# Kernel tuning notes

Measured on AMD Instinct MI355X. Metric: run time of the kernel, lower is better.

## Reference

```python
import jax, jax.numpy as jnp
import numpy as np

B, N, T, H, P = 512, 128, 336, 32, 1  # batch, nodes, seq_len, hidden, pred_len


def setup_inputs() -> dict:
    key = jax.random.key(0)
    ks = jax.random.split(key, 9)
    s = 1.0 / np.sqrt(H)  # torch LSTM/Linear init bound
    u = lambda k, shape: jax.random.uniform(k, shape, dtype=jnp.float32, minval=-s, maxval=s)
    return {
        "x": jax.random.normal(ks[0], (B, N, T), dtype=jnp.float32),
        # layer 0: input_size=1
        "W_ih0": u(ks[1], (N, 4 * H, 1)),
        "W_hh0": u(ks[2], (N, 4 * H, H)),
        "b0": u(ks[3], (N, 4 * H)),  # = b_ih0 + b_hh0 (additive in the cell)
        # layer 1: input_size=H
        "W_ih1": u(ks[4], (N, 4 * H, H)),
        "W_hh1": u(ks[5], (N, 4 * H, H)),
        "b1": u(ks[6], (N, 4 * H)),
        # per-node linear head
        "W_fc": u(ks[7], (N, P, H)),
        "b_fc": u(ks[8], (N, P)),
    }


def _cell(x_proj, h, c, W_hh, b):
    # x_proj, h, c: [B, N, H*(...)]; torch gate order: i, f, g, o
    gates = x_proj + jnp.einsum("bnh,ngh->bng", h, W_hh) + b
    i, f, g, o = jnp.split(gates, 4, axis=-1)
    c = jax.nn.sigmoid(f) * c + jax.nn.sigmoid(i) * jnp.tanh(g)
    h = jax.nn.sigmoid(o) * jnp.tanh(c)
    return h, c


def reference(x, W_ih0, W_hh0, b0, W_ih1, W_hh1, b1, W_fc, b_fc):
    Bx, Nx, Tx = x.shape
    Hx = W_hh0.shape[-1]
    Wi0 = W_ih0[:, :, 0]  # [N, 4H] since input_size == 1
    xs = jnp.moveaxis(x, 2, 0)  # [T, B, N]
    zeros = jnp.zeros((Bx, Nx, Hx), x.dtype)
    init = (zeros, zeros, zeros, zeros)  # h0, c0, h1, c1

    def step(carry, x_t):
        h0, c0, h1, c1 = carry
        xp0 = x_t[:, :, None] * Wi0[None]          # [B, N, 4H]
        h0, c0 = _cell(xp0, h0, c0, W_hh0, b0)
        xp1 = jnp.einsum("bnh,ngh->bng", h0, W_ih1)
        h1, c1 = _cell(xp1, h1, c1, W_hh1, b1)
        return (h0, c0, h1, c1), None

    (h0, c0, h1, c1), _ = jax.lax.scan(step, init, xs)
    # last-timestep top-layer hidden through per-node linear head
    return jnp.einsum("bnh,nph->bnp", h1, W_fc) + b_fc[None]
```

## Files before the change

### kernel.cpp

```cpp
#include <hip/hip_runtime.h>
#include <stdint.h>

#define NB 512
#define NN 128
#define NT 336
#define NH 32
#define NG 128

typedef short bf16x8 __attribute__((ext_vector_type(8)));
typedef float f32x4  __attribute__((ext_vector_type(4)));
typedef float f32x2  __attribute__((ext_vector_type(2)));
typedef float f32v4  __attribute__((ext_vector_type(4)));

#define LOG2E 1.4426950408889634f

__device__ __forceinline__ f32x2 exp2v(f32x2 v) {
  f32x2 r; r.x = __builtin_amdgcn_exp2f(v.x); r.y = __builtin_amdgcn_exp2f(v.y); return r;
}
__device__ __forceinline__ f32x2 rcpv(f32x2 v) {
  f32x2 r; r.x = __builtin_amdgcn_rcpf(v.x); r.y = __builtin_amdgcn_rcpf(v.y); return r;
}
__device__ __forceinline__ short f2bf(float f) {
  unsigned u = __builtin_bit_cast(unsigned, f) + 0x8000u;
  return (short)(u >> 16);
}

template<bool BIAS>
__device__ __forceinline__ f32x2 cell_pair(f32x2 gi, f32x2 gf, f32x2 gg, f32x2 go,
                                           f32x2& cst, float ebi, float ebf,
                                           float ebg, float ebo) {
  f32x2 wi = exp2v(gi), wf = exp2v(gf), uu = exp2v(gg), wo = exp2v(go);
  f32x2 Ai, Af, Au, Ao, nu;
  if (BIAS) {
    Ai = wi * ebi + 1.0f;
    Af = wf * ebf + 1.0f;
    Au = uu * ebg + 1.0f;
    Ao = wo * ebo + 1.0f;
    nu = 1.0f - uu * ebg;
  } else {
    Ai = wi + 1.0f; Af = wf + 1.0f; Au = uu + 1.0f; Ao = wo + 1.0f;
    nu = 1.0f - uu;
  }
  f32x2 P  = Ai * Au;
  f32x2 N  = cst * P + nu * Af;
  f32x2 cn = N * rcpv(Af * P);
  cst = cn;
  f32x2 sarg = cn * (-2.0f * LOG2E);
  sarg.x = fminf(sarg.x, 80.0f);
  sarg.y = fminf(sarg.y, 80.0f);
  f32x2 vv = exp2v(sarg);
  f32x2 hh = (1.0f - vv) * rcpv(Ao * (vv + 1.0f));
  return hh;
}

__global__ __launch_bounds__(256, 2) void lstm_kernel(
    const float* __restrict__ x,
    const float* __restrict__ Wih0,
    const float* __restrict__ Whh0,
    const float* __restrict__ b0,
    const float* __restrict__ Wih1,
    const float* __restrict__ Whh1,
    const float* __restrict__ b1,
    const float* __restrict__ Wfc,
    const float* __restrict__ bfc,
    float* __restrict__ out)
{
  const int tid  = threadIdx.x;
  const int wave = tid >> 6;
  const int lane = tid & 63;
  const int c    = lane & 15;
  const int q    = lane >> 4;
  const int n    = blockIdx.x >> 3;
  const int m0   = ((blockIdx.x & 7) * 4 + wave) * 16;

  __shared__ short lds[4 * 2 * 16 * 40];
  short* my0 = lds + wave * (2 * 16 * 40);
  short* my1 = my0 + 16 * 40;

  const float sc_tab[8] = {-LOG2E, -LOG2E, -LOG2E, -LOG2E,
                           -2.0f * LOG2E, -2.0f * LOG2E, -LOG2E, -LOG2E};

  bf16x8 wb0[8], wb1[8], wb2[8];
  {
    const float* pW0 = Whh0 + n * (NG * NH);
    const float* pW1 = Wih1 + n * (NG * NH);
    const float* pW2 = Whh1 + n * (NG * NH);
#pragma unroll
    for (int tau = 0; tau < 8; ++tau) {
      int off = (tau * 16 + c) * NH + q * 8;
      float sc = sc_tab[tau];
#pragma unroll
      for (int j = 0; j < 8; ++j) {
        wb0[tau][j] = f2bf(sc * pW0[off + j]);
        wb1[tau][j] = f2bf(sc * pW1[off + j]);
        wb2[tau][j] = f2bf(sc * pW2[off + j]);
      }
    }
  }
  float b0g[8], eb1[8], wi0g[8];
#pragma unroll
  for (int tau = 0; tau < 8; ++tau) {
    int g = tau * 16 + c;
    float sc = sc_tab[tau];
    b0g[tau]  = sc * b0[n * NG + g];
    eb1[tau]  = __builtin_amdgcn_exp2f(sc * b1[n * NG + g]);
    wi0g[tau] = sc * Wih0[n * NG + g];
  }
  const float wfc0 = Wfc[n * NH + c];
  const float wfc1 = Wfc[n * NH + 16 + c];

  const float* px0 = x + ((size_t)(m0 + q * 4 + 0) * NN + n) * NT;
  const float* px1 = x + ((size_t)(m0 + q * 4 + 1) * NN + n) * NT;
  const float* px2 = x + ((size_t)(m0 + q * 4 + 2) * NN + n) * NT;
  const float* px3 = x + ((size_t)(m0 + q * 4 + 3) * NN + n) * NT;

  bf16x8 a0 = {0,0,0,0,0,0,0,0};
  bf16x8 a1 = {0,0,0,0,0,0,0,0};
  f32x2 c0p[2][2], c1p[2][2], h1p[2][2];
#pragma unroll
  for (int tu = 0; tu < 2; ++tu)
#pragma unroll
    for (int p = 0; p < 2; ++p) {
      c0p[tu][p] = (f32x2){0.f, 0.f};
      c1p[tu][p] = (f32x2){0.f, 0.f};
      h1p[tu][p] = (f32x2){0.f, 0.f};
    }

  const f32x4 zero4 = {0.f, 0.f, 0.f, 0.f};

#pragma unroll 1
  for (int t4 = 0; t4 < NT / 4; ++t4) {
    f32v4 xr0 = *(const f32v4*)(px0 + t4 * 4);
    f32v4 xr1 = *(const f32v4*)(px1 + t4 * 4);
    f32v4 xr2 = *(const f32v4*)(px2 + t4 * 4);
    f32v4 xr3 = *(const f32v4*)(px3 + t4 * 4);

#pragma unroll
    for (int ts = 0; ts < 4; ++ts) {
      f32x2 x01 = {xr0[ts], xr1[ts]};
      f32x2 x23 = {xr2[ts], xr3[ts]};

      f32x4 acc[8];
#pragma unroll
      for (int tau = 0; tau < 8; ++tau) {
        f32x2 w2 = {wi0g[tau], wi0g[tau]};
        f32x2 b2 = {b0g[tau], b0g[tau]};
        f32x2 lo = x01 * w2 + b2;
        f32x2 hi = x23 * w2 + b2;
        acc[tau] = (f32x4){lo.x, lo.y, hi.x, hi.y};
      }
#pragma unroll
      for (int tau = 0; tau < 8; ++tau)
        acc[tau] = __builtin_amdgcn_mfma_f32_16x16x32_bf16(a0, wb0[tau], acc[tau], 0, 0, 0);

#pragma unroll
      for (int tu = 0; tu < 2; ++tu) {
#pragma unroll
        for (int p = 0; p < 2; ++p) {
          f32x2 gi = { acc[tu    ][2*p], acc[tu    ][2*p+1] };
          f32x2 gf = { acc[tu + 2][2*p], acc[tu + 2][2*p+1] };
          f32x2 gg = { acc[tu + 4][2*p], acc[tu + 4][2*p+1] };
          f32x2 go = { acc[tu + 6][2*p], acc[tu + 6][2*p+1] };
          f32x2 hh = cell_pair<false>(gi, gf, gg, go, c0p[tu][p], 1.f, 1.f, 1.f, 1.f);
          my0[(q * 4 + 2*p    ) * 40 + tu * 16 + c] = f2bf(hh.x);
          my0[(q * 4 + 2*p + 1) * 40 + tu * 16 + c] = f2bf(hh.y);
        }
      }
      asm volatile("" ::: "memory");
      a0 = *(const bf16x8*)(my0 + c * 40 + q * 8);

#pragma unroll
      for (int tau = 0; tau < 8; ++tau)
        acc[tau] = __builtin_amdgcn_mfma_f32_16x16x32_bf16(a0, wb1[tau], zero4, 0, 0, 0);
#pragma unroll
      for (int tau = 0; tau < 8; ++tau)
        acc[tau] = __builtin_amdgcn_mfma_f32_16x16x32_bf16(a1, wb2[tau], acc[tau], 0, 0, 0);

#pragma unroll
      for (int tu = 0; tu < 2; ++tu) {
#pragma unroll
        for (int p = 0; p < 2; ++p) {
          f32x2 gi = { acc[tu    ][2*p], acc[tu    ][2*p+1] };
          f32x2 gf = { acc[tu + 2][2*p], acc[tu + 2][2*p+1] };
          f32x2 gg = { acc[tu + 4][2*p], acc[tu + 4][2*p+1] };
          f32x2 go = { acc[tu + 6][2*p], acc[tu + 6][2*p+1] };
          f32x2 hh = cell_pair<true>(gi, gf, gg, go, c1p[tu][p],
                                     eb1[tu], eb1[tu + 2], eb1[tu + 4], eb1[tu + 6]);
          h1p[tu][p] = hh;
          my1[(q * 4 + 2*p    ) * 40 + tu * 16 + c] = f2bf(hh.x);
          my1[(q * 4 + 2*p + 1) * 40 + tu * 16 + c] = f2bf(hh.y);
        }
      }
      asm volatile("" ::: "memory");
      a1 = *(const bf16x8*)(my1 + c * 40 + q * 8);
    }
  }

  float s0 = h1p[0][0].x * wfc0 + h1p[1][0].x * wfc1;
  float s1 = h1p[0][0].y * wfc0 + h1p[1][0].y * wfc1;
  float s2 = h1p[0][1].x * wfc0 + h1p[1][1].x * wfc1;
  float s3 = h1p[0][1].y * wfc0 + h1p[1][1].y * wfc1;
#pragma unroll
  for (int off = 1; off < 16; off <<= 1) {
    s0 += __shfl_xor(s0, off, 64);
    s1 += __shfl_xor(s1, off, 64);
    s2 += __shfl_xor(s2, off, 64);
    s3 += __shfl_xor(s3, off, 64);
  }
  if (c < 4) {
    float v = (c == 0) ? s0 : (c == 1) ? s1 : (c == 2) ? s2 : s3;
    out[(size_t)(m0 + q * 4 + c) * NN + n] = v + bfc[n];
  }
}

extern "C" void kernel_launch(void* const* d_in, const int* in_sizes, int n_in,
                              void* d_out, int out_size, void* d_ws, size_t ws_size,
                              hipStream_t stream) {
  const float* x    = (const float*)d_in[0];
  const float* Wih0 = (const float*)d_in[1];
  const float* Whh0 = (const float*)d_in[2];
  const float* b0   = (const float*)d_in[3];
  const float* Wih1 = (const float*)d_in[4];
  const float* Whh1 = (const float*)d_in[5];
  const float* b1   = (const float*)d_in[6];
  const float* Wfc  = (const float*)d_in[7];
  const float* bfc  = (const float*)d_in[8];
  float* out = (float*)d_out;

  lstm_kernel<<<dim3(1024), dim3(256), 0, stream>>>(
      x, Wih0, Whh0, b0, Wih1, Whh1, b1, Wfc, bfc, out);
}
```

Measured before the change: 1.301 ms.

## Transpose MFMA operands to keep hidden state in registers, drop LDS round-trip

The recurrent matmuls are reformulated so that weights are the A operand and hidden state the B operand. Each lane's packed bf16 hidden outputs then directly form the next step's operand, which removes the per-step LDS store/load transpose for both layers. The layer-0 input projection and bias are folded into an extra MFMA using split hi/lo bf16 encodings, and the layer-1 bias is used as the accumulator init instead of exp-scaled factors. This adds MFMA work per step and relies on a specific weight K-permutation matching the output layout; correctness depends on that mapping.

Result: slower. 1.329 ms (+2.2%).

```diff
diff --git a/kernel.cpp b/kernel.cpp
--- a/kernel.cpp
+++ b/kernel.cpp
@@ -11,6 +11,7 @@
 typedef float f32x4  __attribute__((ext_vector_type(4)));
 typedef float f32x2  __attribute__((ext_vector_type(2)));
 typedef float f32v4  __attribute__((ext_vector_type(4)));
+typedef unsigned int u32x4 __attribute__((ext_vector_type(4)));
 
 #define LOG2E 1.4426950408889634f
 
@@ -24,23 +25,17 @@
   unsigned u = __builtin_bit_cast(unsigned, f) + 0x8000u;
   return (short)(u >> 16);
 }
-
-template<bool BIAS>
+__device__ __forceinline__ unsigned cvtpk(float a, float b) {
+  unsigned r;
+  asm("v_cvt_pk_bf16_f32 %0, %1, %2" : "=v"(r) : "v"(a), "v"(b));
+  return r;
+}
+
 __device__ __forceinline__ f32x2 cell_pair(f32x2 gi, f32x2 gf, f32x2 gg, f32x2 go,
-                                           f32x2& cst, float ebi, float ebf,
-                                           float ebg, float ebo) {
+                                           f32x2& cst) {
   f32x2 wi = exp2v(gi), wf = exp2v(gf), uu = exp2v(gg), wo = exp2v(go);
-  f32x2 Ai, Af, Au, Ao, nu;
-  if (BIAS) {
-    Ai = wi * ebi + 1.0f;
-    Af = wf * ebf + 1.0f;
-    Au = uu * ebg + 1.0f;
-    Ao = wo * ebo + 1.0f;
-    nu = 1.0f - uu * ebg;
-  } else {
-    Ai = wi + 1.0f; Af = wf + 1.0f; Au = uu + 1.0f; Ao = wo + 1.0f;
-    nu = 1.0f - uu;
-  }
+  f32x2 Ai = wi + 1.0f, Af = wf + 1.0f, Au = uu + 1.0f, Ao = wo + 1.0f;
+  f32x2 nu = 1.0f - uu;
   f32x2 P  = Ai * Au;
   f32x2 N  = cst * P + nu * Af;
   f32x2 cn = N * rcpv(Af * P);
@@ -72,10 +67,7 @@
   const int q    = lane >> 4;
   const int n    = blockIdx.x >> 3;
   const int m0   = ((blockIdx.x & 7) * 4 + wave) * 16;
-
-  __shared__ short lds[4 * 2 * 16 * 40];
-  short* my0 = lds + wave * (2 * 16 * 40);
-  short* my1 = my0 + 16 * 40;
+  const int row  = m0 + c;
 
   const float sc_tab[8] = {-LOG2E, -LOG2E, -LOG2E, -LOG2E,
                            -2.0f * LOG2E, -2.0f * LOG2E, -LOG2E, -LOG2E};
@@ -87,72 +79,89 @@
     const float* pW2 = Whh1 + n * (NG * NH);
 #pragma unroll
     for (int tau = 0; tau < 8; ++tau) {
-      int off = (tau * 16 + c) * NH + q * 8;
       float sc = sc_tab[tau];
+      int rowoff = (tau * 16 + c) * NH;
 #pragma unroll
       for (int j = 0; j < 8; ++j) {
-        wb0[tau][j] = f2bf(sc * pW0[off + j]);
-        wb1[tau][j] = f2bf(sc * pW1[off + j]);
-        wb2[tau][j] = f2bf(sc * pW2[off + j]);
+        int k = (j < 4) ? (q * 4 + j) : (16 + q * 4 + (j - 4));
+        wb0[tau][j] = f2bf(sc * pW0[rowoff + k]);
+        wb1[tau][j] = f2bf(sc * pW1[rowoff + k]);
+        wb2[tau][j] = f2bf(sc * pW2[rowoff + k]);
       }
     }
   }
-  float b0g[8], eb1[8], wi0g[8];
+
+  bf16x8 a2[8];
+  {
+    const bf16x8 z8 = {0,0,0,0,0,0,0,0};
+#pragma unroll
+    for (int tau = 0; tau < 8; ++tau) {
+      float sc = sc_tab[tau];
+      int g = tau * 16 + c;
+      float Wv = sc * Wih0[n * NG + g];
+      unsigned Wb = __builtin_bit_cast(unsigned, Wv) & 0xFFFF0000u;
+      float Bv = sc * b0[n * NG + g];
+      unsigned Bb = __builtin_bit_cast(unsigned, Bv) & 0xFFFF0000u;
+      bf16x8 t;
+      t[0] = (short)(Wb >> 16);
+      t[1] = t[0];
+      t[2] = f2bf(Wv - __builtin_bit_cast(float, Wb));
+      t[3] = (short)(Bb >> 16);
+      t[4] = f2bf(Bv - __builtin_bit_cast(float, Bb));
+      t[5] = 0; t[6] = 0; t[7] = 0;
+      a2[tau] = (q == 0) ? t : z8;
+    }
+  }
+
+  f32x4 b1g4[8];
 #pragma unroll
   for (int tau = 0; tau < 8; ++tau) {
-    int g = tau * 16 + c;
     float sc = sc_tab[tau];
-    b0g[tau]  = sc * b0[n * NG + g];
-    eb1[tau]  = __builtin_amdgcn_exp2f(sc * b1[n * NG + g]);
-    wi0g[tau] = sc * Wih0[n * NG + g];
-  }
-  const float wfc0 = Wfc[n * NH + c];
-  const float wfc1 = Wfc[n * NH + 16 + c];
-
-  const float* px0 = x + ((size_t)(m0 + q * 4 + 0) * NN + n) * NT;
-  const float* px1 = x + ((size_t)(m0 + q * 4 + 1) * NN + n) * NT;
-  const float* px2 = x + ((size_t)(m0 + q * 4 + 2) * NN + n) * NT;
-  const float* px3 = x + ((size_t)(m0 + q * 4 + 3) * NN + n) * NT;
-
-  bf16x8 a0 = {0,0,0,0,0,0,0,0};
-  bf16x8 a1 = {0,0,0,0,0,0,0,0};
-  f32x2 c0p[2][2], c1p[2][2], h1p[2][2];
+#pragma unroll
+    for (int r = 0; r < 4; ++r)
+      b1g4[tau][r] = sc * b1[n * NG + tau * 16 + q * 4 + r];
+  }
+
+  const float* px = x + ((size_t)row * NN + n) * NT;
+
+  bf16x8 h0f = {0,0,0,0,0,0,0,0};
+  bf16x8 h1f = {0,0,0,0,0,0,0,0};
+  f32x2 c0p[2][2], c1p[2][2], h1v[2][2];
 #pragma unroll
   for (int tu = 0; tu < 2; ++tu)
 #pragma unroll
     for (int p = 0; p < 2; ++p) {
       c0p[tu][p] = (f32x2){0.f, 0.f};
       c1p[tu][p] = (f32x2){0.f, 0.f};
-      h1p[tu][p] = (f32x2){0.f, 0.f};
+      h1v[tu][p] = (f32x2){0.f, 0.f};
     }
 
   const f32x4 zero4 = {0.f, 0.f, 0.f, 0.f};
 
 #pragma unroll 1
   for (int t4 = 0; t4 < NT / 4; ++t4) {
-    f32v4 xr0 = *(const f32v4*)(px0 + t4 * 4);
-    f32v4 xr1 = *(const f32v4*)(px1 + t4 * 4);
-    f32v4 xr2 = *(const f32v4*)(px2 + t4 * 4);
-    f32v4 xr3 = *(const f32v4*)(px3 + t4 * 4);
+    f32v4 xr = *(const f32v4*)(px + t4 * 4);
 
 #pragma unroll
     for (int ts = 0; ts < 4; ++ts) {
-      f32x2 x01 = {xr0[ts], xr1[ts]};
-      f32x2 x23 = {xr2[ts], xr3[ts]};
+      float xv = xr[ts];
+      unsigned xb = __builtin_bit_cast(unsigned, xv);
+      unsigned xh = xb & 0xFFFF0000u;
+      float xlf = xv - __builtin_bit_cast(float, xh);
+      unsigned xl = (__builtin_bit_cast(unsigned, xlf) + 0x8000u) & 0xFFFF0000u;
+      unsigned hs = xh >> 16;
+      u32x4 b2w = { hs | xl, hs | 0x3F800000u, 0x00003F80u, 0u };
+      bf16x8 b2 = __builtin_bit_cast(bf16x8, b2w);
 
       f32x4 acc[8];
 #pragma unroll
-      for (int tau = 0; tau < 8; ++tau) {
-        f32x2 w2 = {wi0g[tau], wi0g[tau]};
-        f32x2 b2 = {b0g[tau], b0g[tau]};
-        f32x2 lo = x01 * w2 + b2;
-        f32x2 hi = x23 * w2 + b2;
-        acc[tau] = (f32x4){lo.x, lo.y, hi.x, hi.y};
-      }
-#pragma unroll
-      for (int tau = 0; tau < 8; ++tau)
-        acc[tau] = __builtin_amdgcn_mfma_f32_16x16x32_bf16(a0, wb0[tau], acc[tau], 0, 0, 0);
-
+      for (int tau = 0; tau < 8; ++tau)
+        acc[tau] = __builtin_amdgcn_mfma_f32_16x16x32_bf16(a2[tau], b2, zero4, 0, 0, 0);
+#pragma unroll
+      for (int tau = 0; tau < 8; ++tau)
+        acc[tau] = __builtin_amdgcn_mfma_f32_16x16x32_bf16(wb0[tau], h0f, acc[tau], 0, 0, 0);
+
+      unsigned hd0, hd1, hd2, hd3;
 #pragma unroll
       for (int tu = 0; tu < 2; ++tu) {
 #pragma unroll
@@ -161,20 +170,20 @@
           f32x2 gf = { acc[tu + 2][2*p], acc[tu + 2][2*p+1] };
           f32x2 gg = { acc[tu + 4][2*p], acc[tu + 4][2*p+1] };
           f32x2 go = { acc[tu + 6][2*p], acc[tu + 6][2*p+1] };
-          f32x2 hh = cell_pair<false>(gi, gf, gg, go, c0p[tu][p], 1.f, 1.f, 1.f, 1.f);
-          my0[(q * 4 + 2*p    ) * 40 + tu * 16 + c] = f2bf(hh.x);
-          my0[(q * 4 + 2*p + 1) * 40 + tu * 16 + c] = f2bf(hh.y);
+          f32x2 hh = cell_pair(gi, gf, gg, go, c0p[tu][p]);
+          unsigned d = cvtpk(hh.x, hh.y);
+          if (tu == 0) { if (p == 0) hd0 = d; else hd1 = d; }
+          else         { if (p == 0) hd2 = d; else hd3 = d; }
         }
       }
-      asm volatile("" ::: "memory");
-      a0 = *(const bf16x8*)(my0 + c * 40 + q * 8);
-
-#pragma unroll
-      for (int tau = 0; tau < 8; ++tau)
-        acc[tau] = __builtin_amdgcn_mfma_f32_16x16x32_bf16(a0, wb1[tau], zero4, 0, 0, 0);
-#pragma unroll
-      for (int tau = 0; tau < 8; ++tau)
-        acc[tau] = __builtin_amdgcn_mfma_f32_16x16x32_bf16(a1, wb2[tau], acc[tau], 0, 0, 0);
+      h0f = __builtin_bit_cast(bf16x8, (u32x4){hd0, hd1, hd2, hd3});
+
+#pragma unroll
+      for (int tau = 0; tau < 8; ++tau)
+        acc[tau] = __builtin_amdgcn_mfma_f32_16x16x32_bf16(wb2[tau], h1f, b1g4[tau], 0, 0, 0);
+#pragma unroll
+      for (int tau = 0; tau < 8; ++tau)
+        acc[tau] = __builtin_amdgcn_mfma_f32_16x16x32_bf16(wb1[tau], h0f, acc[tau], 0, 0, 0);
 
 #pragma unroll
       for (int tu = 0; tu < 2; ++tu) {
@@ -184,33 +193,29 @@
           f32x2 gf = { acc[tu + 2][2*p], acc[tu + 2][2*p+1] };
           f32x2 gg = { acc[tu + 4][2*p], acc[tu + 4][2*p+1] };
           f32x2 go = { acc[tu + 6][2*p], acc[tu + 6][2*p+1] };
-          f32x2 hh = cell_pair<true>(gi, gf, gg, go, c1p[tu][p],
-                                     eb1[tu], eb1[tu + 2], eb1[tu + 4], eb1[tu + 6]);
-          h1p[tu][p] = hh;
-          my1[(q * 4 + 2*p    ) * 40 + tu * 16 + c] = f2bf(hh.x);
-          my1[(q * 4 + 2*p + 1) * 40 + tu * 16 + c] = f2bf(hh.y);
+          f32x2 hh = cell_pair(gi, gf, gg, go, c1p[tu][p]);
+          h1v[tu][p] = hh;
+          unsigned d = cvtpk(hh.x, hh.y);
+          if (tu == 0) { if (p == 0) hd0 = d; else hd1 = d; }
+          else         { if (p == 0) hd2 = d; else hd3 = d; }
         }
       }
-      asm volatile("" ::: "memory");
-      a1 = *(const bf16x8*)(my1 + c * 40 + q * 8);
-    }
-  }
-
-  float s0 = h1p[0][0].x * wfc0 + h1p[1][0].x * wfc1;
-  float s1 = h1p[0][0].y * wfc0 + h1p[1][0].y * wfc1;
-  float s2 = h1p[0][1].x * wfc0 + h1p[1][1].x * wfc1;
-  float s3 = h1p[0][1].y * wfc0 + h1p[1][1].y * wfc1;
-#pragma unroll
-  for (int off = 1; off < 16; off <<= 1) {
-    s0 += __shfl_xor(s0, off, 64);
-    s1 += __shfl_xor(s1, off, 64);
-    s2 += __shfl_xor(s2, off, 64);
-    s3 += __shfl_xor(s3, off, 64);
-  }
-  if (c < 4) {
-    float v = (c == 0) ? s0 : (c == 1) ? s1 : (c == 2) ? s2 : s3;
-    out[(size_t)(m0 + q * 4 + c) * NN + n] = v + bfc[n];
-  }
+      h1f = __builtin_bit_cast(bf16x8, (u32x4){hd0, hd1, hd2, hd3});
+    }
+  }
+
+  float s = 0.f;
+#pragma unroll
+  for (int tu = 0; tu < 2; ++tu)
+#pragma unroll
+    for (int p = 0; p < 2; ++p) {
+      int u = tu * 16 + q * 4 + 2 * p;
+      s += h1v[tu][p].x * Wfc[n * NH + u] + h1v[tu][p].y * Wfc[n * NH + u + 1];
+    }
+  s += __shfl_xor(s, 16, 64);
+  s += __shfl_xor(s, 32, 64);
+  if (q == 0)
+    out[(size_t)row * NN + n] = s + bfc[n];
 }
 
 extern "C" void kernel_launch(void* const* d_in, const int* in_sizes, int n_in,
```
